# Kernel optimization log

Measured on AMD Instinct MI355X. Metric: run time of the kernel, lower is better.

Reference implementation:

```python
import jax, jax.numpy as jnp
import numpy as np

B, N, DIN, DINNER, DOUT, W = 4, 8192, 512, 512, 512, 128


def setup_inputs() -> dict:
    key = jax.random.key(0)
    k1, k2, k3 = jax.random.split(key, 3)
    x = jax.random.normal(k1, (B, N, DIN), jnp.float32)
    # torch Linear weights: (out_features, in_features)
    w_qkv = jax.random.normal(k2, (3 * DINNER, DIN), jnp.float32) * (DIN ** -0.5)
    w_out = jax.random.normal(k3, (DOUT, DINNER), jnp.float32) * (DINNER ** -0.5)
    b_out = jnp.zeros((DOUT,), jnp.float32)
    return {"x": x, "w_qkv": w_qkv, "w_out": w_out, "b_out": b_out}


def reference(x, w_qkv, w_out, b_out):
    b, n, _ = x.shape
    w = W
    scale = DINNER ** -0.5
    pad = (-n) % w  # pad_to_multiple along seq dim (static)
    xp = jnp.pad(x, ((0, 0), (0, pad), (0, 0)))
    qkv = jnp.einsum('bnd,ed->bne', xp, w_qkv)  # to_qkv, no bias
    q, k, v = jnp.split(qkv, 3, axis=-1)
    win = lambda t: t.reshape(b, -1, w, DINNER)  # b (w n) d -> b w n d
    q, k, v = win(q), win(k), win(v)
    # prepend one zero bucket to k, then overlap prev/current windows.
    kp = jnp.pad(k, ((0, 0), (1, 0), (0, 0), (0, 0)))
    k2 = jnp.concatenate((kp[:, :-1], kp[:, 1:]), axis=2)  # (b, nb, 2w, d)
    # NOTE: source bug replicated — v is also built from k, not v.
    v2 = jnp.concatenate((kp[:, :-1], kp[:, 1:]), axis=2)
    sim = jnp.einsum('bwid,bwjd->bwij', q, k2) * scale  # (b, nb, w, 2w)
    i, j = w, 2 * w
    mask = jnp.triu(jnp.ones((i, j), bool), j - i + 1)
    sim = jnp.where(mask, -jnp.finfo(sim.dtype).max, sim)
    attn = jax.nn.softmax(sim, axis=-1)
    out = jnp.einsum('bwij,bwjd->bwid', attn, v2)
    out = out.reshape(b, -1, DINNER)[:, :n]
    return jnp.einsum('bnd,od->bno', out, w_out) + b_out
```

## Files before the change

### kernel.cpp

```cpp
#include <hip/hip_runtime.h>
#include <cstdint>
#include <cstddef>

typedef float f32x4 __attribute__((ext_vector_type(4)));
typedef short s16x8 __attribute__((ext_vector_type(8)));
typedef short s16x4 __attribute__((ext_vector_type(4)));

#define MFMA_BF16(a, b, c) __builtin_amdgcn_mfma_f32_16x16x32_bf16((a), (b), (c), 0, 0, 0)

#define GLD16(g, l)                                                            \
  __builtin_amdgcn_global_load_lds(                                            \
      (const __attribute__((address_space(1))) void*)(g),                      \
      (__attribute__((address_space(3))) void*)(l), 16, 0, 0)

__device__ __forceinline__ unsigned short f2bf(float f) {
  unsigned int u = __float_as_uint(f);
  u += 0x7FFFu + ((u >> 16) & 1u);
  return (unsigned short)(u >> 16);
}

__device__ __forceinline__ s16x8 cvt8(const float* __restrict__ src) {
  const float4 f0 = *(const float4*)src;
  const float4 f1 = *(const float4*)(src + 4);
  s16x8 h;
  h[0] = (short)f2bf(f0.x); h[1] = (short)f2bf(f0.y);
  h[2] = (short)f2bf(f0.z); h[3] = (short)f2bf(f0.w);
  h[4] = (short)f2bf(f1.x); h[5] = (short)f2bf(f1.y);
  h[6] = (short)f2bf(f1.z); h[7] = (short)f2bf(f1.w);
  return h;
}

#define XN 16777216
#define WQN 524288
__global__ __launch_bounds__(256)
void cvt_bf16(const float* __restrict__ x, const float* __restrict__ wqkv,
              const float* __restrict__ wout, unsigned short* __restrict__ xb,
              unsigned short* __restrict__ wb, unsigned short* __restrict__ wob) {
  const size_t i = (size_t)(blockIdx.x * 256 + threadIdx.x) * 8;
  const float* src;
  unsigned short* dst;
  if (i < XN) { src = x + i; dst = xb + i; }
  else if (i < XN + WQN) { src = wqkv + (i - XN); dst = wb + (i - XN); }
  else { src = wout + (i - XN - WQN); dst = wob + (i - XN - WQN); }
  *(s16x8*)dst = cvt8(src);
}

__global__ __launch_bounds__(256)
void gemm_qk(const unsigned short* __restrict__ xb, const unsigned short* __restrict__ wb,
             unsigned short* __restrict__ Q, unsigned short* __restrict__ K) {
  __shared__ unsigned short As[2][128 * 64];
  __shared__ unsigned short Bs[2][128 * 64];
  const int t = threadIdx.x, lane = t & 63, wid = t >> 6;
  const int wm = wid >> 1, wn = wid & 1;
  const int nl = lane & 15, quad = lane >> 4;
  const int sub = lane >> 3, lblk = (lane & 7) ^ sub;
  const int l = blockIdx.x;
  const int xcd = l & 7, g = l >> 3;
  const int mt = (g >> 3) * 8 + xcd, nt = g & 7;
  const int m0 = mt * 128, n0 = nt * 128;

  const f32x4 zero = {0.f, 0.f, 0.f, 0.f};
  f32x4 acc[4][4];
#pragma unroll
  for (int i = 0; i < 4; ++i)
#pragma unroll
    for (int j = 0; j < 4; ++j) acc[i][j] = zero;

  const unsigned short* gX = xb + (size_t)(m0 + wid * 32 + sub) * 512 + lblk * 8;
  const unsigned short* gW = wb + (size_t)(n0 + wid * 32 + sub) * 512 + lblk * 8;

#define STAGE_QK(kcc, p)                                                       \
  do {                                                                         \
    _Pragma("unroll") for (int ii = 0; ii < 4; ++ii)                           \
        GLD16(gW + (kcc) + (size_t)(ii * 8) * 512,                             \
              &As[p][(wid * 32 + ii * 8) * 64]);                               \
    _Pragma("unroll") for (int ii = 0; ii < 4; ++ii)                           \
        GLD16(gX + (kcc) + (size_t)(ii * 8) * 512,                             \
              &Bs[p][(wid * 32 + ii * 8) * 64]);                               \
  } while (0)

  STAGE_QK(0, 0);
  for (int s = 0; s < 8; ++s) {
    const int p = s & 1;
    if (s < 7) {
      STAGE_QK((s + 1) * 64, p ^ 1);
      asm volatile("s_waitcnt vmcnt(8)" ::: "memory");
    } else {
      asm volatile("s_waitcnt vmcnt(0)" ::: "memory");
    }
    __builtin_amdgcn_s_barrier();
    asm volatile("" ::: "memory");
    const unsigned short* const asp = As[p];
    const unsigned short* const bsp = Bs[p];
#pragma unroll
    for (int ks = 0; ks < 2; ++ks) {
      s16x8 af[4], bf[4];
#pragma unroll
      for (int i = 0; i < 4; ++i)
        af[i] = *(const s16x8*)&asp[(wm * 64 + i * 16 + nl) * 64 +
                                    (((ks * 4 + quad) ^ (nl & 7)) * 8)];
#pragma unroll
      for (int j = 0; j < 4; ++j)
        bf[j] = *(const s16x8*)&bsp[(wn * 64 + j * 16 + nl) * 64 +
                                    (((ks * 4 + quad) ^ (nl & 7)) * 8)];
      __builtin_amdgcn_s_setprio(1);
#pragma unroll
      for (int i = 0; i < 4; ++i)
#pragma unroll
        for (int j = 0; j < 4; ++j) acc[i][j] = MFMA_BF16(af[i], bf[j], acc[i][j]);
      __builtin_amdgcn_s_setprio(0);
    }
    asm volatile("" ::: "memory");
    __builtin_amdgcn_s_barrier();
  }
#undef STAGE_QK
#pragma unroll
  for (int i = 0; i < 4; ++i) {
    const int n = n0 + wm * 64 + i * 16 + quad * 4;
    unsigned short* base = (n < 512 ? Q : K);
    const int nn = n & 511;
#pragma unroll
    for (int j = 0; j < 4; ++j) {
      const int m = m0 + wn * 64 + j * 16 + nl;
      s16x4 h;
#pragma unroll
      for (int r = 0; r < 4; ++r) h[r] = (short)f2bf(acc[i][j][r]);
      *(s16x4*)&base[(size_t)m * 512 + nn] = h;
    }
  }
}

__global__ __launch_bounds__(256)
void gemm_kwt(const unsigned short* __restrict__ K, const unsigned short* __restrict__ wob,
              unsigned short* __restrict__ KWT) {
  __shared__ unsigned short As[2][128 * 64];
  __shared__ unsigned short Bs[2][128 * 64];
  const int t = threadIdx.x, lane = t & 63, wid = t >> 6;
  const int wm = wid >> 1, wn = wid & 1;
  const int nl = lane & 15, quad = lane >> 4;
  const int sub = lane >> 3, lblk = (lane & 7) ^ sub;
  const int l = blockIdx.x;
  const int xcd = l & 7, g = l >> 3;
  const int mt = (g >> 2) * 8 + xcd, nt = g & 3;
  const int m0 = mt * 128, n0 = nt * 128;

  const f32x4 zero = {0.f, 0.f, 0.f, 0.f};
  f32x4 acc[4][4];
#pragma unroll
  for (int i = 0; i < 4; ++i)
#pragma unroll
    for (int j = 0; j < 4; ++j) acc[i][j] = zero;

  const unsigned short* gA = K + (size_t)(m0 + wid * 32 + sub) * 512 + lblk * 8;
  const unsigned short* gB = wob + (size_t)(n0 + wid * 32 + sub) * 512 + lblk * 8;

#define STAGE_KW(kcc, p)                                                       \
  do {                                                                         \
    _Pragma("unroll") for (int ii = 0; ii < 4; ++ii)                           \
        GLD16(gA + (kcc) + (size_t)(ii * 8) * 512,                             \
              &As[p][(wid * 32 + ii * 8) * 64]);                               \
    _Pragma("unroll") for (int ii = 0; ii < 4; ++ii)                           \
        GLD16(gB + (kcc) + (size_t)(ii * 8) * 512,                             \
              &Bs[p][(wid * 32 + ii * 8) * 64]);                               \
  } while (0)

  STAGE_KW(0, 0);
  for (int s = 0; s < 8; ++s) {
    const int p = s & 1;
    if (s < 7) {
      STAGE_KW((s + 1) * 64, p ^ 1);
      asm volatile("s_waitcnt vmcnt(8)" ::: "memory");
    } else {
      asm volatile("s_waitcnt vmcnt(0)" ::: "memory");
    }
    __builtin_amdgcn_s_barrier();
    asm volatile("" ::: "memory");
    const unsigned short* const asp = As[p];
    const unsigned short* const bsp = Bs[p];
#pragma unroll
    for (int ks = 0; ks < 2; ++ks) {
      s16x8 af[4], bf[4];
#pragma unroll
      for (int i = 0; i < 4; ++i)
        af[i] = *(const s16x8*)&asp[(wm * 64 + i * 16 + nl) * 64 +
                                    (((ks * 4 + quad) ^ (nl & 7)) * 8)];
#pragma unroll
      for (int j = 0; j < 4; ++j)
        bf[j] = *(const s16x8*)&bsp[(wn * 64 + j * 16 + nl) * 64 +
                                    (((ks * 4 + quad) ^ (nl & 7)) * 8)];
      __builtin_amdgcn_s_setprio(1);
#pragma unroll
      for (int i = 0; i < 4; ++i)
#pragma unroll
        for (int j = 0; j < 4; ++j) acc[i][j] = MFMA_BF16(af[i], bf[j], acc[i][j]);
      __builtin_amdgcn_s_setprio(0);
    }
    asm volatile("" ::: "memory");
    __builtin_amdgcn_s_barrier();
  }
#undef STAGE_KW
#pragma unroll
  for (int i = 0; i < 4; ++i) {
    const int ms = m0 + wm * 64 + i * 16 + quad * 4;
    const int b = ms >> 13, ns = ms & 8191;
#pragma unroll
    for (int j = 0; j < 4; ++j) {
      const int o = n0 + wn * 64 + j * 16 + nl;
      s16x4 h;
#pragma unroll
      for (int r = 0; r < 4; ++r) h[r] = (short)f2bf(acc[i][j][r]);
      *(s16x4*)&KWT[(size_t)(b * 512 + o) * 8192 + ns] = h;
    }
  }
}

__global__ __launch_bounds__(256)
void attn64(const unsigned short* __restrict__ Q, const unsigned short* __restrict__ K,
            const unsigned short* __restrict__ KWT, const float* __restrict__ bias,
            float* __restrict__ out) {
  __shared__ __align__(16) char smem[73728];
  unsigned short* const Qb  = (unsigned short*)smem;
  unsigned short* const Kbo = (unsigned short*)(smem + 8192);
  unsigned short* const Kbe = (unsigned short*)(smem + 40960);
  unsigned short* const Ps  = (unsigned short*)smem;
  float* const redm = (float*)(smem + 32768);
  float* const reds = (float*)(smem + 33792);
  unsigned short* const B20 = (unsigned short*)(smem + 40960);
  unsigned short* const B21 = (unsigned short*)(smem + 57344);

  const int t = threadIdx.x, lane = t & 63, wid = t >> 6;
  const int wn = wid;
  const int nl = lane & 15, quad = lane >> 4;
  const int sub = lane >> 3, lblk = (lane & 7) ^ sub;
  const int bx = blockIdx.x;
  const int xcd = bx & 7, half = (bx >> 3) & 1, g = bx >> 4;
  const int wb = g * 8 + xcd, b = wb >> 6, w = wb & 63;

  const unsigned short* Qg = Q + (size_t)(b * 8192 + w * 128 + half * 64) * 512;
  const unsigned short* Kg = K + (size_t)(b * 8192) * 512;
  const unsigned short* KWTb = KWT + (size_t)(b * 512) * 8192;
  const int seqbase = w * 128 - 128;

#define STAGE_Q(kcc)                                                           \
  do {                                                                         \
    _Pragma("unroll") for (int ii = 0; ii < 2; ++ii)                           \
        GLD16(Qg + (size_t)(wid * 16 + ii * 8 + sub) * 512 + (kcc) + lblk * 8, \
              Qb + (wid * 16 + ii * 8) * 64);                                  \
  } while (0)

#define STAGE_K(kcc, kb)                                                       \
  do {                                                                         \
    _Pragma("unroll") for (int ii = 0; ii < 8; ++ii) {                         \
      int sq_ = seqbase + wid * 64 + ii * 8 + sub;                             \
      if (sq_ < 0) sq_ = 0;                                                    \
      GLD16(Kg + (size_t)sq_ * 512 + (kcc) + lblk * 8,                         \
            (kb) + (wid * 64 + ii * 8) * 64);                                  \
    }                                                                          \
  } while (0)

#define STAGE_B2(tt, bb)                                                       \
  do {                                                                         \
    const int och_ = (tt) >> 2, kch_ = (tt) & 3;                               \
    int sq_ = seqbase + kch_ * 64 + lblk * 8;                                  \
    if (sq_ < 0) sq_ = 0;                                                      \
    _Pragma("unroll") for (int ii = 0; ii < 4; ++ii)                           \
        GLD16(KWTb + (size_t)(och_ * 128 + wid * 32 + ii * 8 + sub) * 8192 + sq_, \
              (bb) + (wid * 32 + ii * 8) * 64);                                \
  } while (0)

  float bo[4][2];
#pragma unroll
  for (int och = 0; och < 4; ++och)
#pragma unroll
    for (int j = 0; j < 2; ++j) bo[och][j] = bias[och * 128 + wn * 32 + j * 16 + nl];

  const f32x4 zero = {0.f, 0.f, 0.f, 0.f};
  f32x4 acc[4][4];
#pragma unroll
  for (int i = 0; i < 4; ++i)
#pragma unroll
    for (int j = 0; j < 4; ++j) acc[i][j] = zero;

  STAGE_K(0, Kbe);
  STAGE_Q(0);
#pragma unroll
  for (int s = 0; s < 8; ++s) {
    unsigned short* const kb = (s & 1) ? Kbo : Kbe;
    if (s < 7) {
      STAGE_K((s + 1) * 64, (s & 1) ? Kbe : Kbo);
      asm volatile("s_waitcnt vmcnt(8)" ::: "memory");
    } else {
      STAGE_B2(0, B20);
      asm volatile("s_waitcnt vmcnt(4)" ::: "memory");
    }
    __builtin_amdgcn_s_barrier();
    asm volatile("" ::: "memory");
#pragma unroll
    for (int ks = 0; ks < 2; ++ks) {
      s16x8 af[4], bf[4];
#pragma unroll
      for (int i = 0; i < 4; ++i)
        af[i] = *(const s16x8*)&Qb[(i * 16 + nl) * 64 +
                                   (((ks * 4 + quad) ^ (nl & 7)) * 8)];
#pragma unroll
      for (int j = 0; j < 4; ++j)
        bf[j] = *(const s16x8*)&kb[(wn * 64 + j * 16 + nl) * 64 +
                                   (((ks * 4 + quad) ^ (nl & 7)) * 8)];
      __builtin_amdgcn_s_setprio(1);
#pragma unroll
      for (int i = 0; i < 4; ++i)
#pragma unroll
        for (int j = 0; j < 4; ++j) acc[i][j] = MFMA_BF16(af[i], bf[j], acc[i][j]);
      __builtin_amdgcn_s_setprio(0);
    }
    asm volatile("" ::: "memory");
    __builtin_amdgcn_s_barrier();
    if (s < 7) STAGE_Q((s + 1) * 64);
  }
  STAGE_B2(1, B21);

  const float scale = 0.04419417382415922f;
  float rmax[4][4];
#pragma unroll
  for (int i = 0; i < 4; ++i) {
#pragma unroll
    for (int r = 0; r < 4; ++r) {
      const int qrow = half * 64 + i * 16 + quad * 4 + r;
      float mx = -3.4e38f;
#pragma unroll
      for (int j = 0; j < 4; ++j) {
        const int col = wn * 64 + j * 16 + nl;
        float v = acc[i][j][r] * scale;
        if (col >= 128 && col - 128 > qrow) v = -3.0e38f;
        if (w == 0 && col < 128) v = 0.0f;
        acc[i][j][r] = v;
        mx = fmaxf(mx, v);
      }
      rmax[i][r] = mx;
    }
  }
#pragma unroll
  for (int off = 1; off < 16; off <<= 1)
#pragma unroll
    for (int i = 0; i < 4; ++i)
#pragma unroll
      for (int r = 0; r < 4; ++r)
        rmax[i][r] = fmaxf(rmax[i][r], __shfl_xor(rmax[i][r], off, 64));
  if (nl == 0) {
#pragma unroll
    for (int i = 0; i < 4; ++i)
#pragma unroll
      for (int r = 0; r < 4; ++r)
        redm[(i * 16 + quad * 4 + r) * 4 + wn] = rmax[i][r];
  }
  asm volatile("s_waitcnt lgkmcnt(0)" ::: "memory");
  __builtin_amdgcn_s_barrier();
  asm volatile("" ::: "memory");
  float rsum[4][4];
#pragma unroll
  for (int i = 0; i < 4; ++i) {
#pragma unroll
    for (int r = 0; r < 4; ++r) {
      const f32x4 mv = *(const f32x4*)&redm[(i * 16 + quad * 4 + r) * 4];
      const float m = fmaxf(fmaxf(mv[0], mv[1]), fmaxf(mv[2], mv[3]));
      float s = 0.f;
#pragma unroll
      for (int j = 0; j < 4; ++j) {
        const float p = __expf(acc[i][j][r] - m);
        acc[i][j][r] = p;
        s += p;
      }
      rsum[i][r] = s;
    }
  }
#pragma unroll
  for (int off = 1; off < 16; off <<= 1)
#pragma unroll
    for (int i = 0; i < 4; ++i)
#pragma unroll
      for (int r = 0; r < 4; ++r) rsum[i][r] += __shfl_xor(rsum[i][r], off, 64);
  if (nl == 0) {
#pragma unroll
    for (int i = 0; i < 4; ++i)
#pragma unroll
      for (int r = 0; r < 4; ++r)
        reds[(i * 16 + quad * 4 + r) * 4 + wn] = rsum[i][r];
  }
  asm volatile("s_waitcnt lgkmcnt(0)" ::: "memory");
  __builtin_amdgcn_s_barrier();
  asm volatile("" ::: "memory");
  float invv[4][4];
#pragma unroll
  for (int i = 0; i < 4; ++i)
#pragma unroll
    for (int r = 0; r < 4; ++r) {
      const f32x4 sv = *(const f32x4*)&reds[(i * 16 + quad * 4 + r) * 4];
      invv[i][r] = 1.0f / (sv[0] + sv[1] + sv[2] + sv[3]);
    }
  asm volatile("s_waitcnt lgkmcnt(0)" ::: "memory");
  __builtin_amdgcn_s_barrier();
  asm volatile("" ::: "memory");
#pragma unroll
  for (int i = 0; i < 4; ++i) {
#pragma unroll
    for (int r = 0; r < 4; ++r) {
      const int row = i * 16 + quad * 4 + r;
#pragma unroll
      for (int j = 0; j < 4; ++j) {
        const int col = wn * 64 + j * 16 + nl;
        float pv = acc[i][j][r] * invv[i][r];
        if (w == 0 && col < 128) pv = 0.0f;
        const int cb = col >> 3;
        Ps[row * 256 + (((cb ^ (row & 7)) << 3) | (col & 7))] = f2bf(pv);
      }
    }
  }
  asm volatile("s_waitcnt lgkmcnt(0)" ::: "memory");
  __builtin_amdgcn_s_barrier();
  asm volatile("" ::: "memory");

  f32x4 acc2[4][2];
#pragma unroll
  for (int t2 = 0; t2 < 16; ++t2) {
    const int och = t2 >> 2, kch = t2 & 3;
    unsigned short* const bb = (t2 & 1) ? B21 : B20;
    if (kch == 0) {
#pragma unroll
      for (int i = 0; i < 4; ++i)
#pragma unroll
        for (int j = 0; j < 2; ++j) acc2[i][j] = zero;
    }
    if (t2 < 15) asm volatile("s_waitcnt vmcnt(4)" ::: "memory");
    else         asm volatile("s_waitcnt vmcnt(0)" ::: "memory");
    __builtin_amdgcn_s_barrier();
    asm volatile("" ::: "memory");
#pragma unroll
    for (int ks = 0; ks < 2; ++ks) {
      const int kb2 = kch * 8 + ks * 4 + quad;
      s16x8 af[4], bf[2];
#pragma unroll
      for (int i = 0; i < 4; ++i)
        af[i] = *(const s16x8*)&Ps[(i * 16 + nl) * 256 + ((kb2 ^ (nl & 7)) << 3)];
#pragma unroll
      for (int j = 0; j < 2; ++j)
        bf[j] = *(const s16x8*)&bb[(wn * 32 + j * 16 + nl) * 64 +
                                   (((ks * 4 + quad) ^ (nl & 7)) * 8)];
      __builtin_amdgcn_s_setprio(1);
#pragma unroll
      for (int i = 0; i < 4; ++i) {
        acc2[i][0] = MFMA_BF16(af[i], bf[0], acc2[i][0]);
        acc2[i][1] = MFMA_BF16(af[i], bf[1], acc2[i][1]);
      }
      __builtin_amdgcn_s_setprio(0);
    }
    asm volatile("" ::: "memory");
    __builtin_amdgcn_s_barrier();
    if (kch == 3) {
#pragma unroll
      for (int i = 0; i < 4; ++i) {
        const int seq = w * 128 + half * 64 + i * 16 + quad * 4;
        float* dst = out + (size_t)(b * 8192 + seq) * 512;
#pragma unroll
        for (int j = 0; j < 2; ++j) {
          const int o = och * 128 + wn * 32 + j * 16 + nl;
#pragma unroll
          for (int r = 0; r < 4; ++r) dst[(size_t)r * 512 + o] = acc2[i][j][r] + bo[och][j];
        }
      }
    }
    if (t2 < 14) STAGE_B2(t2 + 2, bb);
  }
#undef STAGE_Q
#undef STAGE_K
#undef STAGE_B2
}

extern "C" void kernel_launch(void* const* d_in, const int* in_sizes, int n_in,
                              void* d_out, int out_size, void* d_ws, size_t ws_size,
                              hipStream_t stream) {
  const float* x = (const float*)d_in[0];
  const float* w_qkv = (const float*)d_in[1];
  const float* w_out = (const float*)d_in[2];
  const float* b_out = (const float*)d_in[3];
  float* out = (float*)d_out;

  char* ws = (char*)d_ws;
  unsigned short* Q = (unsigned short*)ws;
  unsigned short* K = (unsigned short*)(ws + (size_t)33554432);
  unsigned short* xb = (unsigned short*)(ws + (size_t)67108864);
  unsigned short* KWT = (unsigned short*)(ws + (size_t)67108864);
  unsigned short* wb = (unsigned short*)(ws + (size_t)100663296);
  unsigned short* wob = (unsigned short*)(ws + (size_t)100663296 + 1048576);

  cvt_bf16<<<dim3(8576), dim3(256), 0, stream>>>(x, w_qkv, w_out, xb, wb, wob);
  gemm_qk<<<dim3(2048), dim3(256), 0, stream>>>(xb, wb, Q, K);
  gemm_kwt<<<dim3(1024), dim3(256), 0, stream>>>(K, wob, KWT);
  attn64<<<dim3(512), dim3(256), 0, stream>>>(Q, K, KWT, b_out, out);
}
```

Measured before the change: 239.8 us.

## Fuse fp32-to-bf16 conversion of x into the QK projection GEMM

The separate conversion of x to bf16 is removed. The QK GEMM now loads a 32-row fp32 slab of x, converts it into LDS once, and sweeps all Q/K output columns while streaming weight tiles through a double buffer. Only the weights are still pre-converted by a small kernel. This avoids writing and rereading a bf16 copy of x, at the cost of a much smaller M tile, lower weight reuse and heavier L2 traffic for the weights.

Result: slower. 257.6 us (+7.4%).

```diff
diff --git a/kernel.cpp b/kernel.cpp
--- a/kernel.cpp
+++ b/kernel.cpp
@@ -30,104 +30,119 @@
   return h;
 }
 
-#define XN 16777216
+__device__ __forceinline__ s16x8 cvt8r(float4 f0, float4 f1) {
+  s16x8 h;
+  h[0] = (short)f2bf(f0.x); h[1] = (short)f2bf(f0.y);
+  h[2] = (short)f2bf(f0.z); h[3] = (short)f2bf(f0.w);
+  h[4] = (short)f2bf(f1.x); h[5] = (short)f2bf(f1.y);
+  h[6] = (short)f2bf(f1.z); h[7] = (short)f2bf(f1.w);
+  return h;
+}
+
 #define WQN 524288
 __global__ __launch_bounds__(256)
-void cvt_bf16(const float* __restrict__ x, const float* __restrict__ wqkv,
-              const float* __restrict__ wout, unsigned short* __restrict__ xb,
-              unsigned short* __restrict__ wb, unsigned short* __restrict__ wob) {
+void cvt_w(const float* __restrict__ wqkv, const float* __restrict__ wout,
+           unsigned short* __restrict__ wb, unsigned short* __restrict__ wob) {
   const size_t i = (size_t)(blockIdx.x * 256 + threadIdx.x) * 8;
   const float* src;
   unsigned short* dst;
-  if (i < XN) { src = x + i; dst = xb + i; }
-  else if (i < XN + WQN) { src = wqkv + (i - XN); dst = wb + (i - XN); }
-  else { src = wout + (i - XN - WQN); dst = wob + (i - XN - WQN); }
+  if (i < WQN) { src = wqkv + i; dst = wb + i; }
+  else { src = wout + (i - WQN); dst = wob + (i - WQN); }
   *(s16x8*)dst = cvt8(src);
 }
 
 __global__ __launch_bounds__(256)
-void gemm_qk(const unsigned short* __restrict__ xb, const unsigned short* __restrict__ wb,
-             unsigned short* __restrict__ Q, unsigned short* __restrict__ K) {
-  __shared__ unsigned short As[2][128 * 64];
-  __shared__ unsigned short Bs[2][128 * 64];
+void gemm_qk_f(const float* __restrict__ x, const unsigned short* __restrict__ wb,
+               unsigned short* __restrict__ Q, unsigned short* __restrict__ K) {
+  __shared__ __align__(16) unsigned short Xs[8 * 32 * 64];
+  __shared__ __align__(16) unsigned short Ws[2][128 * 64];
   const int t = threadIdx.x, lane = t & 63, wid = t >> 6;
-  const int wm = wid >> 1, wn = wid & 1;
   const int nl = lane & 15, quad = lane >> 4;
   const int sub = lane >> 3, lblk = (lane & 7) ^ sub;
-  const int l = blockIdx.x;
-  const int xcd = l & 7, g = l >> 3;
-  const int mt = (g >> 3) * 8 + xcd, nt = g & 7;
-  const int m0 = mt * 128, n0 = nt * 128;
+  const int m0 = blockIdx.x * 32;
+
+  const int row = t >> 3, cbs = t & 7;
+  float4 rxa[8], rxb[8];
+#pragma unroll
+  for (int c = 0; c < 8; ++c) {
+    const float* p_ = x + (size_t)(m0 + row) * 512 + c * 64 + cbs * 8;
+    rxa[c] = *(const float4*)p_;
+    rxb[c] = *(const float4*)(p_ + 4);
+  }
+  const unsigned short* gW = wb + (size_t)(wid * 32 + sub) * 512 + lblk * 8;
+#define STAGE_W(tln, p)                                                        \
+  do {                                                                         \
+    const int nt_ = (tln) >> 3, kc_ = ((tln) & 7) * 64;                        \
+    _Pragma("unroll") for (int ii = 0; ii < 4; ++ii)                           \
+        GLD16(gW + (size_t)(nt_ * 128 + ii * 8) * 512 + kc_,                   \
+              &Ws[p][(wid * 32 + ii * 8) * 64]);                               \
+  } while (0)
+  STAGE_W(0, 0);
+#pragma unroll
+  for (int c = 0; c < 8; ++c) {
+    *(s16x8*)&Xs[c * 2048 + row * 64 + ((cbs ^ (row & 7)) << 3)] =
+        cvt8r(rxa[c], rxb[c]);
+  }
+  asm volatile("s_waitcnt lgkmcnt(0)" ::: "memory");
+  __builtin_amdgcn_s_barrier();
+  asm volatile("" ::: "memory");
 
   const f32x4 zero = {0.f, 0.f, 0.f, 0.f};
-  f32x4 acc[4][4];
-#pragma unroll
-  for (int i = 0; i < 4; ++i)
-#pragma unroll
-    for (int j = 0; j < 4; ++j) acc[i][j] = zero;
-
-  const unsigned short* gX = xb + (size_t)(m0 + wid * 32 + sub) * 512 + lblk * 8;
-  const unsigned short* gW = wb + (size_t)(n0 + wid * 32 + sub) * 512 + lblk * 8;
-
-#define STAGE_QK(kcc, p)                                                       \
-  do {                                                                         \
-    _Pragma("unroll") for (int ii = 0; ii < 4; ++ii)                           \
-        GLD16(gW + (kcc) + (size_t)(ii * 8) * 512,                             \
-              &As[p][(wid * 32 + ii * 8) * 64]);                               \
-    _Pragma("unroll") for (int ii = 0; ii < 4; ++ii)                           \
-        GLD16(gX + (kcc) + (size_t)(ii * 8) * 512,                             \
-              &Bs[p][(wid * 32 + ii * 8) * 64]);                               \
-  } while (0)
-
-  STAGE_QK(0, 0);
-  for (int s = 0; s < 8; ++s) {
-    const int p = s & 1;
-    if (s < 7) {
-      STAGE_QK((s + 1) * 64, p ^ 1);
-      asm volatile("s_waitcnt vmcnt(8)" ::: "memory");
-    } else {
-      asm volatile("s_waitcnt vmcnt(0)" ::: "memory");
-    }
-    __builtin_amdgcn_s_barrier();
-    asm volatile("" ::: "memory");
-    const unsigned short* const asp = As[p];
-    const unsigned short* const bsp = Bs[p];
-#pragma unroll
-    for (int ks = 0; ks < 2; ++ks) {
-      s16x8 af[4], bf[4];
-#pragma unroll
-      for (int i = 0; i < 4; ++i)
-        af[i] = *(const s16x8*)&asp[(wm * 64 + i * 16 + nl) * 64 +
-                                    (((ks * 4 + quad) ^ (nl & 7)) * 8)];
-#pragma unroll
-      for (int j = 0; j < 4; ++j)
-        bf[j] = *(const s16x8*)&bsp[(wn * 64 + j * 16 + nl) * 64 +
-                                    (((ks * 4 + quad) ^ (nl & 7)) * 8)];
-      __builtin_amdgcn_s_setprio(1);
-#pragma unroll
-      for (int i = 0; i < 4; ++i)
-#pragma unroll
-        for (int j = 0; j < 4; ++j) acc[i][j] = MFMA_BF16(af[i], bf[j], acc[i][j]);
-      __builtin_amdgcn_s_setprio(0);
-    }
-    asm volatile("" ::: "memory");
-    __builtin_amdgcn_s_barrier();
-  }
-#undef STAGE_QK
-#pragma unroll
-  for (int i = 0; i < 4; ++i) {
-    const int n = n0 + wm * 64 + i * 16 + quad * 4;
-    unsigned short* base = (n < 512 ? Q : K);
-    const int nn = n & 511;
-#pragma unroll
-    for (int j = 0; j < 4; ++j) {
-      const int m = m0 + wn * 64 + j * 16 + nl;
-      s16x4 h;
-#pragma unroll
-      for (int r = 0; r < 4; ++r) h[r] = (short)f2bf(acc[i][j][r]);
-      *(s16x4*)&base[(size_t)m * 512 + nn] = h;
-    }
-  }
+  f32x4 acc[2][2];
+#pragma unroll
+  for (int i = 0; i < 2; ++i)
+#pragma unroll
+    for (int j = 0; j < 2; ++j) acc[i][j] = zero;
+
+  for (int nt = 0; nt < 8; ++nt) {
+#pragma unroll
+    for (int kcs = 0; kcs < 8; ++kcs) {
+      const int tl = nt * 8 + kcs;
+      const int p = kcs & 1;
+      if (tl < 63) {
+        STAGE_W(tl + 1, p ^ 1);
+        asm volatile("s_waitcnt vmcnt(4)" ::: "memory");
+      } else {
+        asm volatile("s_waitcnt vmcnt(0)" ::: "memory");
+      }
+      const unsigned short* const wsp = Ws[p];
+      const unsigned short* const xsp = &Xs[kcs * 2048];
+#pragma unroll
+      for (int ks = 0; ks < 2; ++ks) {
+        s16x8 af[2], bf[2];
+#pragma unroll
+        for (int i = 0; i < 2; ++i)
+          af[i] = *(const s16x8*)&wsp[(wid * 32 + i * 16 + nl) * 64 +
+                                      (((ks * 4 + quad) ^ (nl & 7)) * 8)];
+#pragma unroll
+        for (int j = 0; j < 2; ++j)
+          bf[j] = *(const s16x8*)&xsp[(j * 16 + nl) * 64 +
+                                      (((ks * 4 + quad) ^ (nl & 7)) * 8)];
+        __builtin_amdgcn_s_setprio(1);
+#pragma unroll
+        for (int i = 0; i < 2; ++i)
+#pragma unroll
+          for (int j = 0; j < 2; ++j) acc[i][j] = MFMA_BF16(af[i], bf[j], acc[i][j]);
+        __builtin_amdgcn_s_setprio(0);
+      }
+    }
+#pragma unroll
+    for (int i = 0; i < 2; ++i) {
+      const int n = nt * 128 + wid * 32 + i * 16 + quad * 4;
+      unsigned short* base = (n < 512 ? Q : K);
+      const int nn = n & 511;
+#pragma unroll
+      for (int j = 0; j < 2; ++j) {
+        const int m = m0 + j * 16 + nl;
+        s16x4 h;
+#pragma unroll
+        for (int r = 0; r < 4; ++r) h[r] = (short)f2bf(acc[i][j][r]);
+        *(s16x4*)&base[(size_t)m * 512 + nn] = h;
+        acc[i][j] = zero;
+      }
+    }
+  }
+#undef STAGE_W
 }
 
 __global__ __launch_bounds__(256)
@@ -487,13 +502,12 @@
   char* ws = (char*)d_ws;
   unsigned short* Q = (unsigned short*)ws;
   unsigned short* K = (unsigned short*)(ws + (size_t)33554432);
-  unsigned short* xb = (unsigned short*)(ws + (size_t)67108864);
   unsigned short* KWT = (unsigned short*)(ws + (size_t)67108864);
   unsigned short* wb = (unsigned short*)(ws + (size_t)100663296);
   unsigned short* wob = (unsigned short*)(ws + (size_t)100663296 + 1048576);
 
-  cvt_bf16<<<dim3(8576), dim3(256), 0, stream>>>(x, w_qkv, w_out, xb, wb, wob);
-  gemm_qk<<<dim3(2048), dim3(256), 0, stream>>>(xb, wb, Q, K);
+  cvt_w<<<dim3(384), dim3(256), 0, stream>>>(w_qkv, w_out, wb, wob);
+  gemm_qk_f<<<dim3(1024), dim3(256), 0, stream>>>(x, wb, Q, K);
   gemm_kwt<<<dim3(1024), dim3(256), 0, stream>>>(K, wob, KWT);
   attn64<<<dim3(512), dim3(256), 0, stream>>>(Q, K, KWT, b_out, out);
 }
```
